# Kernel tuning notes

Measured on AMD Instinct MI355X. Metric: run time of the kernel, lower is better.

Reference implementation:

```python
import jax, jax.numpy as jnp
import numpy as np

N, HID, HEADS = 50000, 256, 8
D = HID // HEADS  # per-head dim = 32
E = 800000


def setup_inputs() -> dict:
    key = jax.random.key(0)
    ks = jax.random.split(key, 12)
    s = 0.02
    x = jax.random.normal(ks[0], (N, HID), dtype=jnp.float32)
    edge_index = jax.random.randint(ks[1], (2, E), 0, N, dtype=jnp.int64)
    # TransformerConv params (PyG defaults: root_weight=True, concat=True, beta=False)
    Wq = jax.random.normal(ks[2], (HID, HID), dtype=jnp.float32) * s
    bq = jnp.zeros((HID,), dtype=jnp.float32)
    Wk = jax.random.normal(ks[3], (HID, HID), dtype=jnp.float32) * s
    bk = jnp.zeros((HID,), dtype=jnp.float32)
    Wv = jax.random.normal(ks[4], (HID, HID), dtype=jnp.float32) * s
    bv = jnp.zeros((HID,), dtype=jnp.float32)
    Wskip = jax.random.normal(ks[5], (HID, HID), dtype=jnp.float32) * s
    bskip = jnp.zeros((HID,), dtype=jnp.float32)
    gamma = jnp.ones((HID,), dtype=jnp.float32)
    beta = jnp.zeros((HID,), dtype=jnp.float32)
    return {"x": x, "edge_index": edge_index, "Wq": Wq, "bq": bq, "Wk": Wk,
            "bk": bk, "Wv": Wv, "bv": bv, "Wskip": Wskip, "bskip": bskip,
            "gamma": gamma, "beta": beta}


def _gnn_layer(x, edge_index, Wq, bq, Wk, bk, Wv, bv, Wskip, bskip, gamma, beta):
    n = x.shape[0]
    src, dst = edge_index[0], edge_index[1]  # messages flow src(j) -> dst(i)
    q = (x @ Wq + bq).reshape(n, HEADS, D)
    k = (x @ Wk + bk).reshape(n, HEADS, D)
    v = (x @ Wv + bv).reshape(n, HEADS, D)
    # per-edge attention logits [E, HEADS]
    logits = jnp.einsum('ehd,ehd->eh', q[dst], k[src]) / jnp.sqrt(jnp.float32(D))
    # segment softmax over destination neighborhoods (stable)
    seg_max = jax.ops.segment_max(logits, dst, num_segments=n)  # [N, HEADS]
    expv = jnp.exp(logits - seg_max[dst])
    denom = jax.ops.segment_sum(expv, dst, num_segments=n)
    attn = expv / denom[dst]  # [E, HEADS]  (dropout in eval mode -> identity)
    # scatter-aggregate weighted values, concat heads
    agg = jax.ops.segment_sum(attn[:, :, None] * v[src], dst, num_segments=n)
    out = agg.reshape(n, HID) + (x @ Wskip + bskip)  # root/skip connection
    h = jax.nn.gelu(out, approximate=False)
    # residual + LayerNorm
    y = x + h
    mu = jnp.mean(y, axis=-1, keepdims=True)
    var = jnp.var(y, axis=-1, keepdims=True)
    return (y - mu) / jnp.sqrt(var + 1e-5) * gamma + beta


def reference(x, edge_index, Wq, bq, Wk, bk, Wv, bv, Wskip, bskip, gamma, beta):
    return _gnn_layer(x, edge_index, Wq, bq, Wk, bk, Wv, bv, Wskip, bskip, gamma, beta)
```

## Files before the change

kernel.cpp:

```cpp
#include <hip/hip_runtime.h>

#define N_NODES 50000
#define HID 256
#define HEADS 8
#define HDIM 32
#define N_EDGES 800000

typedef __bf16 bf16x8 __attribute__((ext_vector_type(8)));
typedef float f32x4 __attribute__((ext_vector_type(4)));
typedef float f32x2 __attribute__((ext_vector_type(2)));

__device__ __forceinline__ unsigned short f2bf(float f) {
    unsigned int b = __float_as_uint(f);
    unsigned int r = (b + 0x7FFFu + ((b >> 16) & 1u)) >> 16;
    return (unsigned short)r;
}
__device__ __forceinline__ float bf2f(unsigned short u) {
    return __uint_as_float(((unsigned int)u) << 16);
}
__device__ __forceinline__ f32x2 bfpair(unsigned int u) {
    f32x2 r;
    r[0] = __uint_as_float(u << 16);
    r[1] = __uint_as_float(u & 0xffff0000u);
    return r;
}

__global__ __launch_bounds__(256) void prep_kernel(
    const float* __restrict__ x, unsigned short* __restrict__ xb,
    const int* __restrict__ dst, int* __restrict__ deg) {
    int b = blockIdx.x;
    if (b < 6250) {
        int t = b * 256 + threadIdx.x;
        const float4* p = reinterpret_cast<const float4*>(x) + (size_t)t * 2;
        float4 f0 = p[0], f1 = p[1];
        uint4 o;
        o.x = (unsigned)f2bf(f0.x) | ((unsigned)f2bf(f0.y) << 16);
        o.y = (unsigned)f2bf(f0.z) | ((unsigned)f2bf(f0.w) << 16);
        o.z = (unsigned)f2bf(f1.x) | ((unsigned)f2bf(f1.y) << 16);
        o.w = (unsigned)f2bf(f1.z) | ((unsigned)f2bf(f1.w) << 16);
        reinterpret_cast<uint4*>(xb)[t] = o;
    } else {
        int e = (b - 6250) * 256 + threadIdx.x;
        atomicAdd(&deg[dst[e]], 1);
    }
}

__device__ __forceinline__ void fused_col_map(int p, int& mat, int& col, float& scale) {
    if (p < 256) { mat = 0; col = p; scale = 1.0f; }
    else if (p < 768) {
        int pp = p - 256;
        mat = ((pp & 2) ? 2 : 1);
        col = ((pp >> 2) << 1) | (pp & 1);
        scale = 64.0f;
    } else { mat = 3; col = p - 768; scale = 1.0f; }
}

__global__ __launch_bounds__(256) void pack_w_kernel(
    const float* __restrict__ Wq, const float* __restrict__ Wk,
    const float* __restrict__ Wv, const float* __restrict__ Ws,
    const float* __restrict__ bq, const float* __restrict__ bk,
    const float* __restrict__ bv, const float* __restrict__ bs,
    unsigned short* __restrict__ wpack, float* __restrict__ biasF) {
    int t = blockIdx.x * 256 + threadIdx.x;
    int e = t & 7, lane = (t >> 3) & 63, kk = (t >> 9) & 7, n_tile = t >> 12;
    int k = kk * 32 + (lane >> 4) * 8 + e;
    int p = n_tile * 16 + (lane & 15);
    const float* W[4] = {Wq, Wk, Wv, Ws};
    int mat, col; float scale;
    fused_col_map(p, mat, col, scale);
    wpack[t] = f2bf(W[mat][k * 256 + col] * scale);
    if (t < 1024) {
        const float* B[4] = {bq, bk, bv, bs};
        int mat2, col2; float s2;
        fused_col_map(t, mat2, col2, s2);
        biasF[t] = B[mat2][col2] * s2;
    }
}

__global__ __launch_bounds__(1024) void scan1_kernel(
    const int* __restrict__ deg, int* __restrict__ row_ptr,
    int* __restrict__ btot, int n) {
    int tid = threadIdx.x, lane = tid & 63, wv = tid >> 6;
    int idx = blockIdx.x * 1024 + tid;
    int v = (idx < n) ? deg[idx] : 0;
    int inc = v;
#pragma unroll
    for (int off = 1; off < 64; off <<= 1) {
        int t2 = __shfl_up(inc, off);
        if (lane >= off) inc += t2;
    }
    __shared__ int sW[16], sO[16];
    if (lane == 63) sW[wv] = inc;
    __syncthreads();
    if (tid < 16) {
        int vv = sW[tid], in2 = vv;
        for (int off = 1; off < 16; off <<= 1) {
            int t2 = __shfl_up(in2, off);
            if (tid >= off) in2 += t2;
        }
        sO[tid] = in2 - vv;
    }
    __syncthreads();
    int excl = sO[wv] + inc - v;
    if (idx <= n) row_ptr[idx] = excl;
    if (tid == 1023) btot[blockIdx.x] = excl + v;
}

__global__ __launch_bounds__(64) void scan2_kernel(
    const int* __restrict__ btot, int* __restrict__ boff, int nb) {
    int t = threadIdx.x;
    int v = (t < nb) ? btot[t] : 0;
    int inc = v;
#pragma unroll
    for (int off = 1; off < 64; off <<= 1) {
        int t2 = __shfl_up(inc, off);
        if (t >= off) inc += t2;
    }
    if (t < nb) boff[t] = inc - v;
}

__global__ __launch_bounds__(256) void fixup_kernel(
    int* __restrict__ row_ptr, int* __restrict__ fill,
    const int* __restrict__ boff, int n) {
    int idx = blockIdx.x * 256 + threadIdx.x;
    if (idx > n) return;
    int v = row_ptr[idx] + boff[idx >> 10];
    row_ptr[idx] = v;
    if (idx < n) fill[idx] = v;
}

__global__ __launch_bounds__(256) void scatter_kernel(
    const int* __restrict__ src, const int* __restrict__ dst,
    int* __restrict__ fill, int* __restrict__ csr_src, int ne) {
    int e = blockIdx.x * 256 + threadIdx.x;
    if (e < ne) {
        int pos = atomicAdd(&fill[dst[e]], 1);
        csr_src[pos] = src[e];
    }
}

__global__ __launch_bounds__(256) void gemm_kernel(
    const unsigned short* __restrict__ xb,
    const unsigned short* __restrict__ wpack,
    const float* __restrict__ biasF,
    unsigned char* __restrict__ qkvs,
    int n_nodes) {
    int bid = blockIdx.x;
    int work = (bid & 7) * 782 + (bid >> 3);
    int mt = work >> 4;
    int nt = work & 15;
    int lane = threadIdx.x & 63;
    int wv = threadIdx.x >> 6;
    int row_w = mt * 128 + wv * 32;
    int n0 = nt * 64;

    f32x4 acc[2][4];
#pragma unroll
    for (int mi = 0; mi < 2; ++mi)
#pragma unroll
        for (int ni = 0; ni < 4; ++ni) {
            f32x4 z = {0.f, 0.f, 0.f, 0.f};
            acc[mi][ni] = z;
        }

    int arow0 = min(row_w + (lane & 15), n_nodes - 1);
    int arow1 = min(row_w + 16 + (lane & 15), n_nodes - 1);
    int acol = (lane >> 4) * 8;
    const uint4* bbase = reinterpret_cast<const uint4*>(wpack);
    int ntile0 = n0 >> 4;

#pragma unroll
    for (int kk = 0; kk < 8; ++kk) {
        bf16x8 a[2], b[4];
        {
            uint4 u0 = *reinterpret_cast<const uint4*>(xb + (size_t)arow0 * 256 + kk * 32 + acol);
            uint4 u1 = *reinterpret_cast<const uint4*>(xb + (size_t)arow1 * 256 + kk * 32 + acol);
            a[0] = __builtin_bit_cast(bf16x8, u0);
            a[1] = __builtin_bit_cast(bf16x8, u1);
        }
#pragma unroll
        for (int ni = 0; ni < 4; ++ni) {
            uint4 u = bbase[((size_t)(ntile0 + ni) * 8 + kk) * 64 + lane];
            b[ni] = __builtin_bit_cast(bf16x8, u);
        }
#pragma unroll
        for (int mi = 0; mi < 2; ++mi)
#pragma unroll
            for (int ni = 0; ni < 4; ++ni)
                acc[mi][ni] = __builtin_amdgcn_mfma_f32_16x16x32_bf16(a[mi], b[ni], acc[mi][ni], 0, 0, 0);
    }

    int region = (n0 < 256) ? 0 : (n0 < 768 ? 1 : 2);
#pragma unroll
    for (int mi = 0; mi < 2; ++mi) {
        int rbase = row_w + mi * 16 + (lane >> 4) * 4;
#pragma unroll
        for (int ni = 0; ni < 4; ++ni) {
            int col = n0 + ni * 16 + (lane & 15);
            float bias = biasF[col];
#pragma unroll
            for (int r = 0; r < 4; ++r) {
                int row = rbase + r;
                if (row < n_nodes) {
                    float val = acc[mi][ni][r] + bias;
                    size_t rb = (size_t)row * 1536;
                    if (region == 0) {
                        *reinterpret_cast<unsigned short*>(qkvs + rb + col * 2) = f2bf(val);
                    } else if (region == 1) {
                        int p8 = __builtin_amdgcn_cvt_pk_fp8_f32(val, val, 0, false);
                        qkvs[rb + 512 + (col - 256)] = (unsigned char)(p8 & 0xff);
                    } else {
                        *reinterpret_cast<unsigned short*>(qkvs + rb + 1024 + (col - 768) * 2) = f2bf(val);
                    }
                }
            }
        }
    }
}

__global__ __launch_bounds__(256) void edge_agg_kernel(
    const int* __restrict__ row_ptr, const int* __restrict__ csr_src,
    const unsigned char* __restrict__ qkvs, const unsigned short* __restrict__ xb,
    const float* __restrict__ gamma, const float* __restrict__ beta,
    float* __restrict__ out) {
    int wv = threadIdx.x >> 6;
    int i = blockIdx.x * 4 + wv;
    int lane = threadIdx.x & 63;
    int half = lane >> 5, l = lane & 31;

    const float QS = 0.17677669529663687f * 1.4426950408889634f / 64.0f;
    const unsigned char* rowi = qkvs + (unsigned)i * 1536u;
    uint4 qu = *reinterpret_cast<const uint4*>(rowi + l * 16);
    f32x2 qsc = {QS, QS};
    f32x2 q01 = bfpair(qu.x) * qsc;
    f32x2 q23 = bfpair(qu.y) * qsc;
    f32x2 q45 = bfpair(qu.z) * qsc;
    f32x2 q67 = bfpair(qu.w) * qsc;

    int e0 = row_ptr[i], e1 = row_ptr[i + 1];
    f32x2 acc0 = {0.f, 0.f}, acc1 = {0.f, 0.f}, acc2 = {0.f, 0.f}, acc3 = {0.f, 0.f};
    float den = 0.f;
    int e = e0 + half;
    int j = (e < e1) ? csr_src[e] : 0;
    while (e < e1) {
        int jn = (e + 2 < e1) ? csr_src[e + 2] : 0;
        uint4 u = *reinterpret_cast<const uint4*>(
            qkvs + (unsigned)j * 1536u + 512u + (unsigned)l * 16u);
        f32x2 k01 = __builtin_amdgcn_cvt_pk_f32_fp8(u.x, false);
        f32x2 v01 = __builtin_amdgcn_cvt_pk_f32_fp8(u.x, true);
        f32x2 k23 = __builtin_amdgcn_cvt_pk_f32_fp8(u.y, false);
        f32x2 v23 = __builtin_amdgcn_cvt_pk_f32_fp8(u.y, true);
        f32x2 k45 = __builtin_amdgcn_cvt_pk_f32_fp8(u.z, false);
        f32x2 v45 = __builtin_amdgcn_cvt_pk_f32_fp8(u.z, true);
        f32x2 k67 = __builtin_amdgcn_cvt_pk_f32_fp8(u.w, false);
        f32x2 v67 = __builtin_amdgcn_cvt_pk_f32_fp8(u.w, true);
        f32x2 d = q01 * k01;
        d = __builtin_elementwise_fma(q23, k23, d);
        d = __builtin_elementwise_fma(q45, k45, d);
        d = __builtin_elementwise_fma(q67, k67, d);
        float s = d[0] + d[1];
        s += __shfl_xor(s, 1);
        s += __shfl_xor(s, 2);
        float w = exp2f(s);
        den += w;
        f32x2 w2 = {w, w};
        acc0 = __builtin_elementwise_fma(w2, v01, acc0);
        acc1 = __builtin_elementwise_fma(w2, v23, acc1);
        acc2 = __builtin_elementwise_fma(w2, v45, acc2);
        acc3 = __builtin_elementwise_fma(w2, v67, acc3);
        j = jn;
        e += 2;
    }

    acc0[0] += __shfl_xor(acc0[0], 32); acc0[1] += __shfl_xor(acc0[1], 32);
    acc1[0] += __shfl_xor(acc1[0], 32); acc1[1] += __shfl_xor(acc1[1], 32);
    acc2[0] += __shfl_xor(acc2[0], 32); acc2[1] += __shfl_xor(acc2[1], 32);
    acc3[0] += __shfl_xor(acc3[0], 32); acc3[1] += __shfl_xor(acc3[1], 32);
    den += __shfl_xor(den, 32);
    float inv = (den > 0.f) ? 1.0f / (den * 64.0f) : 0.f;

    uint4 su = *reinterpret_cast<const uint4*>(rowi + 1024 + l * 16);
    uint4 xu = *reinterpret_cast<const uint4*>(
        reinterpret_cast<const unsigned char*>(xb) + (unsigned)i * 512u + l * 16);
    const float C1 = -2.3022650556f;
    const float C2 = -0.10294578f;
    float s1 = 0.f, s2 = 0.f;
    f32x2 y01, y23, y45, y67;
#define GNN_PROC(A, SRAW, XRAW, Y)                                   \
    {                                                                \
        f32x2 sk = bfpair(SRAW), xr = bfpair(XRAW);                  \
        _Pragma("unroll")                                            \
        for (int qq = 0; qq < 2; ++qq) {                             \
            float pre = fmaf(A[qq], inv, sk[qq]);                    \
            float x2 = pre * pre;                                    \
            float arg = pre * fmaf(C2, x2, C1);                      \
            float gel = pre / (1.f + exp2f(arg));                    \
            float yy = xr[qq] + gel;                                 \
            Y[qq] = yy;                                              \
            s1 += yy;                                                \
            s2 = fmaf(yy, yy, s2);                                   \
        }                                                            \
    }
    GNN_PROC(acc0, su.x, xu.x, y01)
    GNN_PROC(acc1, su.y, xu.y, y23)
    GNN_PROC(acc2, su.z, xu.z, y45)
    GNN_PROC(acc3, su.w, xu.w, y67)
#undef GNN_PROC

#pragma unroll
    for (int m = 1; m <= 16; m <<= 1) {
        s1 += __shfl_xor(s1, m);
        s2 += __shfl_xor(s2, m);
    }
    float mu = s1 * (1.f / 256.f);
    float var = s2 * (1.f / 256.f) - mu * mu;
    float rstd = rsqrtf(var + 1e-5f);

    if (half == 0) {
        const float4* g4 = reinterpret_cast<const float4*>(gamma) + l * 2;
        const float4* b4 = reinterpret_cast<const float4*>(beta) + l * 2;
        float4 ga = g4[0], gb = g4[1], ba = b4[0], bb = b4[1];
        float4 o0, o1;
        o0.x = (y01[0] - mu) * rstd * ga.x + ba.x;
        o0.y = (y01[1] - mu) * rstd * ga.y + ba.y;
        o0.z = (y23[0] - mu) * rstd * ga.z + ba.z;
        o0.w = (y23[1] - mu) * rstd * ga.w + ba.w;
        o1.x = (y45[0] - mu) * rstd * gb.x + bb.x;
        o1.y = (y45[1] - mu) * rstd * gb.y + bb.y;
        o1.z = (y67[0] - mu) * rstd * gb.z + bb.z;
        o1.w = (y67[1] - mu) * rstd * gb.w + bb.w;
        float4* op = reinterpret_cast<float4*>(out + (unsigned)i * 256u + l * 8);
        op[0] = o0;
        op[1] = o1;
    }
}

extern "C" void kernel_launch(void* const* d_in, const int* in_sizes, int n_in,
                              void* d_out, int out_size, void* d_ws, size_t ws_size,
                              hipStream_t stream) {
    const float* x    = (const float*)d_in[0];
    const int*   ei   = (const int*)d_in[1];
    const float* Wq   = (const float*)d_in[2];
    const float* bq   = (const float*)d_in[3];
    const float* Wk   = (const float*)d_in[4];
    const float* bk   = (const float*)d_in[5];
    const float* Wv   = (const float*)d_in[6];
    const float* bv   = (const float*)d_in[7];
    const float* Wsk  = (const float*)d_in[8];
    const float* bsk  = (const float*)d_in[9];
    const float* gamma = (const float*)d_in[10];
    const float* beta  = (const float*)d_in[11];
    const int* src = ei;
    const int* dst = ei + N_EDGES;

    char* ws = (char*)d_ws;
    size_t off = 0;
    auto alloc = [&](size_t bytes) -> void* {
        void* p = ws + off;
        off += (bytes + 255) & ~(size_t)255;
        return p;
    };
    unsigned short* xb     = (unsigned short*)alloc((size_t)N_NODES * 256 * 2);
    unsigned char*  qkvs   = (unsigned char*)alloc((size_t)N_NODES * 1536);
    unsigned short* wpack  = (unsigned short*)alloc(262144 * 2);
    float*          biasF  = (float*)alloc(1024 * 4);
    int*            deg    = (int*)alloc((size_t)N_NODES * 4);
    int*            rowp   = (int*)alloc((size_t)(N_NODES + 1) * 4);
    int*            fill   = (int*)alloc((size_t)N_NODES * 4);
    int*            csr    = (int*)alloc((size_t)N_EDGES * 4);
    int*            btot   = (int*)alloc(64 * 4);
    int*            boff   = (int*)alloc(64 * 4);
    (void)ws_size;

    hipMemsetAsync(deg, 0, (size_t)N_NODES * 4, stream);
    prep_kernel<<<9375, 256, 0, stream>>>(x, xb, dst, deg);
    pack_w_kernel<<<1024, 256, 0, stream>>>(Wq, Wk, Wv, Wsk, bq, bk, bv, bsk, wpack, biasF);
    scan1_kernel<<<50, 1024, 0, stream>>>(deg, rowp, btot, N_NODES);
    scan2_kernel<<<1, 64, 0, stream>>>(btot, boff, 50);
    fixup_kernel<<<196, 256, 0, stream>>>(rowp, fill, boff, N_NODES);
    scatter_kernel<<<3125, 256, 0, stream>>>(src, dst, fill, csr, N_EDGES);
    gemm_kernel<<<6256, 256, 0, stream>>>(xb, wpack, biasF, qkvs, N_NODES);
    edge_agg_kernel<<<12500, 256, 0, stream>>>(rowp, csr, qkvs, xb, gamma, beta, (float*)d_out);
}
```

Measured before the change: 265.9 us.

## Enlarge GEMM wave tile, prefetch operands, vectorize stores into split Q/KV/skip buffers

The projection GEMM now computes a 64x64 tile per wave instead of 32x64, with the weight and activation operands swapped so each lane holds four consecutive output columns. Operand fragments are double-buffered in registers so the loads for the next k-step overlap the current MFMAs. Stores become packed 8-byte bf16 or 4-byte fp8 writes into separate Q, KV and skip arrays, replacing scattered 2-byte and 1-byte stores into one interleaved buffer. The edge kernel is updated to read the new layouts. The larger tile and the prefetch buffers raise register pressure, which may lower occupancy.

Result: slower. 276.7 us (+4.1%).

```diff
diff --git a/kernel.cpp b/kernel.cpp
--- a/kernel.cpp
+++ b/kernel.cpp
@@ -143,75 +143,94 @@
     const unsigned short* __restrict__ xb,
     const unsigned short* __restrict__ wpack,
     const float* __restrict__ biasF,
-    unsigned char* __restrict__ qkvs,
+    unsigned short* __restrict__ qs,
+    unsigned char* __restrict__ kv,
+    unsigned short* __restrict__ sk,
     int n_nodes) {
     int bid = blockIdx.x;
-    int work = (bid & 7) * 782 + (bid >> 3);
-    int mt = work >> 4;
-    int nt = work & 15;
+    int work = (bid & 7) * 392 + (bid >> 3);
+    int rt = work >> 4;
+    int ct = work & 15;
     int lane = threadIdx.x & 63;
     int wv = threadIdx.x >> 6;
-    int row_w = mt * 128 + wv * 32;
-    int n0 = nt * 64;
-
-    f32x4 acc[2][4];
-#pragma unroll
-    for (int mi = 0; mi < 2; ++mi)
-#pragma unroll
-        for (int ni = 0; ni < 4; ++ni) {
+    int rbase = rt * 256 + wv * 64;
+    int n0 = ct * 64;
+    int ntile0 = n0 >> 4;
+
+    f32x4 acc[4][4];
+#pragma unroll
+    for (int cf = 0; cf < 4; ++cf)
+#pragma unroll
+        for (int rf = 0; rf < 4; ++rf) {
             f32x4 z = {0.f, 0.f, 0.f, 0.f};
-            acc[mi][ni] = z;
+            acc[cf][rf] = z;
         }
 
-    int arow0 = min(row_w + (lane & 15), n_nodes - 1);
-    int arow1 = min(row_w + 16 + (lane & 15), n_nodes - 1);
-    int acol = (lane >> 4) * 8;
+    int xrow[4];
+#pragma unroll
+    for (int rf = 0; rf < 4; ++rf)
+        xrow[rf] = min(rbase + rf * 16 + (lane & 15), n_nodes - 1);
+    int xcol = (lane >> 4) * 8;
     const uint4* bbase = reinterpret_cast<const uint4*>(wpack);
-    int ntile0 = n0 >> 4;
+
+    uint4 wf[2][4], xf[2][4];
+#pragma unroll
+    for (int cf = 0; cf < 4; ++cf)
+        wf[0][cf] = bbase[(size_t)((ntile0 + cf) * 8 + 0) * 64 + lane];
+#pragma unroll
+    for (int rf = 0; rf < 4; ++rf)
+        xf[0][rf] = *reinterpret_cast<const uint4*>(xb + (size_t)xrow[rf] * 256 + xcol);
 
 #pragma unroll
     for (int kk = 0; kk < 8; ++kk) {
-        bf16x8 a[2], b[4];
-        {
-            uint4 u0 = *reinterpret_cast<const uint4*>(xb + (size_t)arow0 * 256 + kk * 32 + acol);
-            uint4 u1 = *reinterpret_cast<const uint4*>(xb + (size_t)arow1 * 256 + kk * 32 + acol);
-            a[0] = __builtin_bit_cast(bf16x8, u0);
-            a[1] = __builtin_bit_cast(bf16x8, u1);
+        int cur = kk & 1, nxt = cur ^ 1;
+        if (kk < 7) {
+#pragma unroll
+            for (int cf = 0; cf < 4; ++cf)
+                wf[nxt][cf] = bbase[(size_t)((ntile0 + cf) * 8 + kk + 1) * 64 + lane];
+#pragma unroll
+            for (int rf = 0; rf < 4; ++rf)
+                xf[nxt][rf] = *reinterpret_cast<const uint4*>(
+                    xb + (size_t)xrow[rf] * 256 + (kk + 1) * 32 + xcol);
         }
 #pragma unroll
-        for (int ni = 0; ni < 4; ++ni) {
-            uint4 u = bbase[((size_t)(ntile0 + ni) * 8 + kk) * 64 + lane];
-            b[ni] = __builtin_bit_cast(bf16x8, u);
-        }
-#pragma unroll
-        for (int mi = 0; mi < 2; ++mi)
-#pragma unroll
-            for (int ni = 0; ni < 4; ++ni)
-                acc[mi][ni] = __builtin_amdgcn_mfma_f32_16x16x32_bf16(a[mi], b[ni], acc[mi][ni], 0, 0, 0);
+        for (int cf = 0; cf < 4; ++cf)
+#pragma unroll
+            for (int rf = 0; rf < 4; ++rf)
+                acc[cf][rf] = __builtin_amdgcn_mfma_f32_16x16x32_bf16(
+                    __builtin_bit_cast(bf16x8, wf[cur][cf]),
+                    __builtin_bit_cast(bf16x8, xf[cur][rf]), acc[cf][rf], 0, 0, 0);
     }
 
     int region = (n0 < 256) ? 0 : (n0 < 768 ? 1 : 2);
-#pragma unroll
-    for (int mi = 0; mi < 2; ++mi) {
-        int rbase = row_w + mi * 16 + (lane >> 4) * 4;
-#pragma unroll
-        for (int ni = 0; ni < 4; ++ni) {
-            int col = n0 + ni * 16 + (lane & 15);
-            float bias = biasF[col];
-#pragma unroll
-            for (int r = 0; r < 4; ++r) {
-                int row = rbase + r;
-                if (row < n_nodes) {
-                    float val = acc[mi][ni][r] + bias;
-                    size_t rb = (size_t)row * 1536;
-                    if (region == 0) {
-                        *reinterpret_cast<unsigned short*>(qkvs + rb + col * 2) = f2bf(val);
-                    } else if (region == 1) {
-                        int p8 = __builtin_amdgcn_cvt_pk_fp8_f32(val, val, 0, false);
-                        qkvs[rb + 512 + (col - 256)] = (unsigned char)(p8 & 0xff);
-                    } else {
-                        *reinterpret_cast<unsigned short*>(qkvs + rb + 1024 + (col - 768) * 2) = f2bf(val);
-                    }
+    int pbase = n0 + (lane >> 4) * 4;
+#pragma unroll
+    for (int cf = 0; cf < 4; ++cf) {
+        int p0 = pbase + cf * 16;
+        float4 b4 = *reinterpret_cast<const float4*>(biasF + p0);
+#pragma unroll
+        for (int rf = 0; rf < 4; ++rf) {
+            int rr = rbase + rf * 16 + (lane & 15);
+            if (rr < n_nodes) {
+                float v0 = acc[cf][rf][0] + b4.x;
+                float v1 = acc[cf][rf][1] + b4.y;
+                float v2 = acc[cf][rf][2] + b4.z;
+                float v3 = acc[cf][rf][3] + b4.w;
+                if (region == 0) {
+                    uint2 o;
+                    o.x = (unsigned)f2bf(v0) | ((unsigned)f2bf(v1) << 16);
+                    o.y = (unsigned)f2bf(v2) | ((unsigned)f2bf(v3) << 16);
+                    *reinterpret_cast<uint2*>(qs + (size_t)rr * 256 + p0) = o;
+                } else if (region == 1) {
+                    int d = __builtin_amdgcn_cvt_pk_fp8_f32(v0, v1, 0, false);
+                    d = __builtin_amdgcn_cvt_pk_fp8_f32(v2, v3, d, true);
+                    *reinterpret_cast<unsigned int*>(kv + (size_t)rr * 512 + (p0 - 256)) =
+                        (unsigned)d;
+                } else {
+                    uint2 o;
+                    o.x = (unsigned)f2bf(v0) | ((unsigned)f2bf(v1) << 16);
+                    o.y = (unsigned)f2bf(v2) | ((unsigned)f2bf(v3) << 16);
+                    *reinterpret_cast<uint2*>(sk + (size_t)rr * 256 + (p0 - 768)) = o;
                 }
             }
         }
@@ -220,7 +239,8 @@
 
 __global__ __launch_bounds__(256) void edge_agg_kernel(
     const int* __restrict__ row_ptr, const int* __restrict__ csr_src,
-    const unsigned char* __restrict__ qkvs, const unsigned short* __restrict__ xb,
+    const unsigned short* __restrict__ qs, const unsigned char* __restrict__ kv,
+    const unsigned short* __restrict__ sk, const unsigned short* __restrict__ xb,
     const float* __restrict__ gamma, const float* __restrict__ beta,
     float* __restrict__ out) {
     int wv = threadIdx.x >> 6;
@@ -229,8 +249,7 @@
     int half = lane >> 5, l = lane & 31;
 
     const float QS = 0.17677669529663687f * 1.4426950408889634f / 64.0f;
-    const unsigned char* rowi = qkvs + (unsigned)i * 1536u;
-    uint4 qu = *reinterpret_cast<const uint4*>(rowi + l * 16);
+    uint4 qu = *reinterpret_cast<const uint4*>(qs + (size_t)i * 256 + l * 8);
     f32x2 qsc = {QS, QS};
     f32x2 q01 = bfpair(qu.x) * qsc;
     f32x2 q23 = bfpair(qu.y) * qsc;
@@ -245,7 +264,7 @@
     while (e < e1) {
         int jn = (e + 2 < e1) ? csr_src[e + 2] : 0;
         uint4 u = *reinterpret_cast<const uint4*>(
-            qkvs + (unsigned)j * 1536u + 512u + (unsigned)l * 16u);
+            kv + (size_t)j * 512u + (unsigned)l * 16u);
         f32x2 k01 = __builtin_amdgcn_cvt_pk_f32_fp8(u.x, false);
         f32x2 v01 = __builtin_amdgcn_cvt_pk_f32_fp8(u.x, true);
         f32x2 k23 = __builtin_amdgcn_cvt_pk_f32_fp8(u.y, false);
@@ -279,19 +298,18 @@
     den += __shfl_xor(den, 32);
     float inv = (den > 0.f) ? 1.0f / (den * 64.0f) : 0.f;
 
-    uint4 su = *reinterpret_cast<const uint4*>(rowi + 1024 + l * 16);
-    uint4 xu = *reinterpret_cast<const uint4*>(
-        reinterpret_cast<const unsigned char*>(xb) + (unsigned)i * 512u + l * 16);
+    uint4 su = *reinterpret_cast<const uint4*>(sk + (size_t)i * 256 + l * 8);
+    uint4 xu = *reinterpret_cast<const uint4*>(xb + (size_t)i * 256 + l * 8);
     const float C1 = -2.3022650556f;
     const float C2 = -0.10294578f;
     float s1 = 0.f, s2 = 0.f;
     f32x2 y01, y23, y45, y67;
 #define GNN_PROC(A, SRAW, XRAW, Y)                                   \
     {                                                                \
-        f32x2 sk = bfpair(SRAW), xr = bfpair(XRAW);                  \
+        f32x2 skp = bfpair(SRAW), xr = bfpair(XRAW);                 \
         _Pragma("unroll")                                            \
         for (int qq = 0; qq < 2; ++qq) {                             \
-            float pre = fmaf(A[qq], inv, sk[qq]);                    \
+            float pre = fmaf(A[qq], inv, skp[qq]);                   \
             float x2 = pre * pre;                                    \
             float arg = pre * fmaf(C2, x2, C1);                      \
             float gel = pre / (1.f + exp2f(arg));                    \
@@ -329,7 +347,7 @@
         o1.y = (y45[1] - mu) * rstd * gb.y + bb.y;
         o1.z = (y67[0] - mu) * rstd * gb.z + bb.z;
         o1.w = (y67[1] - mu) * rstd * gb.w + bb.w;
-        float4* op = reinterpret_cast<float4*>(out + (unsigned)i * 256u + l * 8);
+        float4* op = reinterpret_cast<float4*>(out + (size_t)i * 256 + l * 8);
         op[0] = o0;
         op[1] = o1;
     }
@@ -361,7 +379,9 @@
         return p;
     };
     unsigned short* xb     = (unsigned short*)alloc((size_t)N_NODES * 256 * 2);
-    unsigned char*  qkvs   = (unsigned char*)alloc((size_t)N_NODES * 1536);
+    unsigned short* qs     = (unsigned short*)alloc((size_t)N_NODES * 256 * 2);
+    unsigned char*  kvb    = (unsigned char*)alloc((size_t)N_NODES * 512);
+    unsigned short* sk     = (unsigned short*)alloc((size_t)N_NODES * 256 * 2);
     unsigned short* wpack  = (unsigned short*)alloc(262144 * 2);
     float*          biasF  = (float*)alloc(1024 * 4);
     int*            deg    = (int*)alloc((size_t)N_NODES * 4);
@@ -379,6 +399,7 @@
     scan2_kernel<<<1, 64, 0, stream>>>(btot, boff, 50);
     fixup_kernel<<<196, 256, 0, stream>>>(rowp, fill, boff, N_NODES);
     scatter_kernel<<<3125, 256, 0, stream>>>(src, dst, fill, csr, N_EDGES);
-    gemm_kernel<<<6256, 256, 0, stream>>>(xb, wpack, biasF, qkvs, N_NODES);
-    edge_agg_kernel<<<12500, 256, 0, stream>>>(rowp, csr, qkvs, xb, gamma, beta, (float*)d_out);
-}
+    gemm_kernel<<<3136, 256, 0, stream>>>(xb, wpack, biasF, qs, kvb, sk, N_NODES);
+    edge_agg_kernel<<<12500, 256, 0, stream>>>(rowp, csr, qs, kvb, sk, xb, gamma, beta,
+                                               (float*)d_out);
+}
```

## Merge small launches: fold weight packing, block scan, and scatter into neighbors

Applied to the files above, without the earlier changes.

Folds the weight/bias packing into the prep kernel as extra blocks, moves the 50-entry block-offset scan into each fixup block, and runs the CSR scatter and the QKV GEMM as disjoint block ranges of one launch. This removes three kernel launches and the serialization gaps between them, and lets the scatter's atomics overlap with GEMM compute. In exchange, every fixup block redundantly rescans the block totals, and the fused kernel's register and occupancy footprint is set by the GEMM path even for scatter blocks.

New measurement: 258.1 us. 1.03x faster.

```diff
diff --git a/kernel.cpp b/kernel.cpp
--- a/kernel.cpp
+++ b/kernel.cpp
@@ -25,9 +25,24 @@
     return r;
 }
 
+__device__ __forceinline__ void fused_col_map(int p, int& mat, int& col, float& scale) {
+    if (p < 256) { mat = 0; col = p; scale = 1.0f; }
+    else if (p < 768) {
+        int pp = p - 256;
+        mat = ((pp & 2) ? 2 : 1);
+        col = ((pp >> 2) << 1) | (pp & 1);
+        scale = 64.0f;
+    } else { mat = 3; col = p - 768; scale = 1.0f; }
+}
+
 __global__ __launch_bounds__(256) void prep_kernel(
     const float* __restrict__ x, unsigned short* __restrict__ xb,
-    const int* __restrict__ dst, int* __restrict__ deg) {
+    const int* __restrict__ dst, int* __restrict__ deg,
+    const float* __restrict__ Wq, const float* __restrict__ Wk,
+    const float* __restrict__ Wv, const float* __restrict__ Ws,
+    const float* __restrict__ bq, const float* __restrict__ bk,
+    const float* __restrict__ bv, const float* __restrict__ bs,
+    unsigned short* __restrict__ wpack, float* __restrict__ biasF) {
     int b = blockIdx.x;
     if (b < 6250) {
         int t = b * 256 + threadIdx.x;
@@ -39,41 +54,24 @@
         o.z = (unsigned)f2bf(f1.x) | ((unsigned)f2bf(f1.y) << 16);
         o.w = (unsigned)f2bf(f1.z) | ((unsigned)f2bf(f1.w) << 16);
         reinterpret_cast<uint4*>(xb)[t] = o;
-    } else {
+    } else if (b < 9375) {
         int e = (b - 6250) * 256 + threadIdx.x;
         atomicAdd(&deg[dst[e]], 1);
-    }
-}
-
-__device__ __forceinline__ void fused_col_map(int p, int& mat, int& col, float& scale) {
-    if (p < 256) { mat = 0; col = p; scale = 1.0f; }
-    else if (p < 768) {
-        int pp = p - 256;
-        mat = ((pp & 2) ? 2 : 1);
-        col = ((pp >> 2) << 1) | (pp & 1);
-        scale = 64.0f;
-    } else { mat = 3; col = p - 768; scale = 1.0f; }
-}
-
-__global__ __launch_bounds__(256) void pack_w_kernel(
-    const float* __restrict__ Wq, const float* __restrict__ Wk,
-    const float* __restrict__ Wv, const float* __restrict__ Ws,
-    const float* __restrict__ bq, const float* __restrict__ bk,
-    const float* __restrict__ bv, const float* __restrict__ bs,
-    unsigned short* __restrict__ wpack, float* __restrict__ biasF) {
-    int t = blockIdx.x * 256 + threadIdx.x;
-    int e = t & 7, lane = (t >> 3) & 63, kk = (t >> 9) & 7, n_tile = t >> 12;
-    int k = kk * 32 + (lane >> 4) * 8 + e;
-    int p = n_tile * 16 + (lane & 15);
-    const float* W[4] = {Wq, Wk, Wv, Ws};
-    int mat, col; float scale;
-    fused_col_map(p, mat, col, scale);
-    wpack[t] = f2bf(W[mat][k * 256 + col] * scale);
-    if (t < 1024) {
-        const float* B[4] = {bq, bk, bv, bs};
-        int mat2, col2; float s2;
-        fused_col_map(t, mat2, col2, s2);
-        biasF[t] = B[mat2][col2] * s2;
+    } else {
+        int t = (b - 9375) * 256 + threadIdx.x;
+        int e = t & 7, lane = (t >> 3) & 63, kk = (t >> 9) & 7, n_tile = t >> 12;
+        int k = kk * 32 + (lane >> 4) * 8 + e;
+        int p = n_tile * 16 + (lane & 15);
+        const float* W[4] = {Wq, Wk, Wv, Ws};
+        int mat, col; float scale;
+        fused_col_map(p, mat, col, scale);
+        wpack[t] = f2bf(W[mat][k * 256 + col] * scale);
+        if (t < 1024) {
+            const float* B[4] = {bq, bk, bv, bs};
+            int mat2, col2; float s2;
+            fused_col_map(t, mat2, col2, s2);
+            biasF[t] = B[mat2][col2] * s2;
+        }
     }
 }
 
@@ -106,47 +104,48 @@
     if (tid == 1023) btot[blockIdx.x] = excl + v;
 }
 
-__global__ __launch_bounds__(64) void scan2_kernel(
-    const int* __restrict__ btot, int* __restrict__ boff, int nb) {
-    int t = threadIdx.x;
-    int v = (t < nb) ? btot[t] : 0;
-    int inc = v;
-#pragma unroll
-    for (int off = 1; off < 64; off <<= 1) {
-        int t2 = __shfl_up(inc, off);
-        if (t >= off) inc += t2;
-    }
-    if (t < nb) boff[t] = inc - v;
-}
-
 __global__ __launch_bounds__(256) void fixup_kernel(
     int* __restrict__ row_ptr, int* __restrict__ fill,
-    const int* __restrict__ boff, int n) {
-    int idx = blockIdx.x * 256 + threadIdx.x;
+    const int* __restrict__ btot, int n) {
+    __shared__ int sB;
+    int tid = threadIdx.x;
+    if (tid < 64) {
+        int v = (tid < 50) ? btot[tid] : 0;
+        int inc = v;
+#pragma unroll
+        for (int off = 1; off < 64; off <<= 1) {
+            int t2 = __shfl_up(inc, off);
+            if (tid >= off) inc += t2;
+        }
+        if (tid == (blockIdx.x >> 2)) sB = inc - v;
+    }
+    __syncthreads();
+    int idx = blockIdx.x * 256 + tid;
     if (idx > n) return;
-    int v = row_ptr[idx] + boff[idx >> 10];
+    int v = row_ptr[idx] + sB;
     row_ptr[idx] = v;
     if (idx < n) fill[idx] = v;
 }
 
-__global__ __launch_bounds__(256) void scatter_kernel(
+__global__ __launch_bounds__(256) void gemm_scatter_kernel(
     const int* __restrict__ src, const int* __restrict__ dst,
-    int* __restrict__ fill, int* __restrict__ csr_src, int ne) {
-    int e = blockIdx.x * 256 + threadIdx.x;
-    if (e < ne) {
-        int pos = atomicAdd(&fill[dst[e]], 1);
-        csr_src[pos] = src[e];
-    }
-}
-
-__global__ __launch_bounds__(256) void gemm_kernel(
+    int* __restrict__ fill, int* __restrict__ csr_src,
     const unsigned short* __restrict__ xb,
     const unsigned short* __restrict__ wpack,
     const float* __restrict__ biasF,
     unsigned char* __restrict__ qkvs,
     int n_nodes) {
-    int bid = blockIdx.x;
-    int work = (bid & 7) * 782 + (bid >> 3);
+    int b = blockIdx.x;
+    if (b < 3125) {
+        int e = b * 256 + threadIdx.x;
+        if (e < N_EDGES) {
+            int pos = atomicAdd(&fill[dst[e]], 1);
+            csr_src[pos] = src[e];
+        }
+        return;
+    }
+    int gid = b - 3125;
+    int work = (gid & 7) * 782 + (gid >> 3);
     int mt = work >> 4;
     int nt = work & 15;
     int lane = threadIdx.x & 63;
@@ -171,7 +170,7 @@
 
 #pragma unroll
     for (int kk = 0; kk < 8; ++kk) {
-        bf16x8 a[2], b[4];
+        bf16x8 a[2], bfr[4];
         {
             uint4 u0 = *reinterpret_cast<const uint4*>(xb + (size_t)arow0 * 256 + kk * 32 + acol);
             uint4 u1 = *reinterpret_cast<const uint4*>(xb + (size_t)arow1 * 256 + kk * 32 + acol);
@@ -181,13 +180,14 @@
 #pragma unroll
         for (int ni = 0; ni < 4; ++ni) {
             uint4 u = bbase[((size_t)(ntile0 + ni) * 8 + kk) * 64 + lane];
-            b[ni] = __builtin_bit_cast(bf16x8, u);
+            bfr[ni] = __builtin_bit_cast(bf16x8, u);
         }
 #pragma unroll
         for (int mi = 0; mi < 2; ++mi)
 #pragma unroll
             for (int ni = 0; ni < 4; ++ni)
-                acc[mi][ni] = __builtin_amdgcn_mfma_f32_16x16x32_bf16(a[mi], b[ni], acc[mi][ni], 0, 0, 0);
+                acc[mi][ni] = __builtin_amdgcn_mfma_f32_16x16x32_bf16(
+                    a[mi], bfr[ni], acc[mi][ni], 0, 0, 0);
     }
 
     int region = (n0 < 256) ? 0 : (n0 < 768 ? 1 : 2);
@@ -280,18 +280,17 @@
     float inv = (den > 0.f) ? 1.0f / (den * 64.0f) : 0.f;
 
     uint4 su = *reinterpret_cast<const uint4*>(rowi + 1024 + l * 16);
-    uint4 xu = *reinterpret_cast<const uint4*>(
-        reinterpret_cast<const unsigned char*>(xb) + (unsigned)i * 512u + l * 16);
+    uint4 xu = *reinterpret_cast<const uint4*>(xb + (size_t)i * 256 + l * 8);
     const float C1 = -2.3022650556f;
     const float C2 = -0.10294578f;
     float s1 = 0.f, s2 = 0.f;
     f32x2 y01, y23, y45, y67;
 #define GNN_PROC(A, SRAW, XRAW, Y)                                   \
     {                                                                \
-        f32x2 sk = bfpair(SRAW), xr = bfpair(XRAW);                  \
+        f32x2 skp = bfpair(SRAW), xr = bfpair(XRAW);                 \
         _Pragma("unroll")                                            \
         for (int qq = 0; qq < 2; ++qq) {                             \
-            float pre = fmaf(A[qq], inv, sk[qq]);                    \
+            float pre = fmaf(A[qq], inv, skp[qq]);                   \
             float x2 = pre * pre;                                    \
             float arg = pre * fmaf(C2, x2, C1);                      \
             float gel = pre / (1.f + exp2f(arg));                    \
@@ -369,16 +368,15 @@
     int*            fill   = (int*)alloc((size_t)N_NODES * 4);
     int*            csr    = (int*)alloc((size_t)N_EDGES * 4);
     int*            btot   = (int*)alloc(64 * 4);
-    int*            boff   = (int*)alloc(64 * 4);
     (void)ws_size;
 
     hipMemsetAsync(deg, 0, (size_t)N_NODES * 4, stream);
-    prep_kernel<<<9375, 256, 0, stream>>>(x, xb, dst, deg);
-    pack_w_kernel<<<1024, 256, 0, stream>>>(Wq, Wk, Wv, Wsk, bq, bk, bv, bsk, wpack, biasF);
+    prep_kernel<<<10399, 256, 0, stream>>>(x, xb, dst, deg, Wq, Wk, Wv, Wsk,
+                                           bq, bk, bv, bsk, wpack, biasF);
     scan1_kernel<<<50, 1024, 0, stream>>>(deg, rowp, btot, N_NODES);
-    scan2_kernel<<<1, 64, 0, stream>>>(btot, boff, 50);
-    fixup_kernel<<<196, 256, 0, stream>>>(rowp, fill, boff, N_NODES);
-    scatter_kernel<<<3125, 256, 0, stream>>>(src, dst, fill, csr, N_EDGES);
-    gemm_kernel<<<6256, 256, 0, stream>>>(xb, wpack, biasF, qkvs, N_NODES);
-    edge_agg_kernel<<<12500, 256, 0, stream>>>(rowp, csr, qkvs, xb, gamma, beta, (float*)d_out);
-}
+    fixup_kernel<<<196, 256, 0, stream>>>(rowp, fill, btot, N_NODES);
+    gemm_scatter_kernel<<<9381, 256, 0, stream>>>(src, dst, fill, csr,
+                                                  xb, wpack, biasF, qkvs, N_NODES);
+    edge_agg_kernel<<<12500, 256, 0, stream>>>(rowp, csr, qkvs, xb, gamma, beta,
+                                               (float*)d_out);
+}
```
